# Performance work log

Measured on AMD Instinct MI355X. Metric: run time of the kernel, lower is better.

Reference implementation:

```python
import jax, jax.numpy as jnp
import numpy as np

NUM_SEQS = 64
NUM_HEADS = 32
NUM_KV_HEADS = 8
HEAD_DIM = 128
BLOCK_SIZE = 16
MAX_SEQLEN_K = 1024
BLOCKS_PER_SEQ = MAX_SEQLEN_K // BLOCK_SIZE  # 64
NUM_BLOCKS = NUM_SEQS * BLOCKS_PER_SEQ      # 4096
SCALE = 1.0 / float(np.sqrt(HEAD_DIM))
EPS = 1e-6
ROPE_BASE = 10000.0


def setup_inputs() -> dict:
    key = jax.random.key(0)
    ks = jax.random.split(key, 8)
    q = jax.random.normal(ks[0], (NUM_SEQS, NUM_HEADS * HEAD_DIM), jnp.float32)
    k = jax.random.normal(ks[1], (NUM_SEQS, NUM_KV_HEADS * HEAD_DIM), jnp.float32)
    v = jax.random.normal(ks[2], (NUM_SEQS, NUM_KV_HEADS * HEAD_DIM), jnp.float32)
    k_cache = jax.random.normal(ks[3], (NUM_BLOCKS, BLOCK_SIZE, NUM_KV_HEADS, HEAD_DIM), jnp.float32)
    v_cache = jax.random.normal(ks[4], (NUM_BLOCKS, BLOCK_SIZE, NUM_KV_HEADS, HEAD_DIM), jnp.float32)
    qw = 1.0 + 0.1 * jax.random.normal(ks[5], (HEAD_DIM,), jnp.float32)
    kw = 1.0 + 0.1 * jax.random.normal(ks[6], (HEAD_DIM,), jnp.float32)
    # neox rotary cos/sin caches over half the head dim
    inv_freq = 1.0 / (ROPE_BASE ** (jnp.arange(0, HEAD_DIM, 2, dtype=jnp.float32) / HEAD_DIM))
    ang = jnp.arange(MAX_SEQLEN_K, dtype=jnp.float32)[:, None] * inv_freq[None, :]  # [S_max, D/2]
    cos_cache = jnp.cos(ang)
    sin_cache = jnp.sin(ang)
    # decode step: each seq has context_lens tokens already; new token at position context_lens-1
    context_lens = jax.random.randint(ks[7], (NUM_SEQS,), MAX_SEQLEN_K // 2, MAX_SEQLEN_K + 1).astype(jnp.int32)
    position = context_lens - 1
    block_tables = jnp.arange(NUM_SEQS * BLOCKS_PER_SEQ, dtype=jnp.int32).reshape(NUM_SEQS, BLOCKS_PER_SEQ)
    slot_mapping = jnp.arange(NUM_SEQS, dtype=jnp.int32) * MAX_SEQLEN_K + position
    return dict(q=q, k=k, v=v, k_cache=k_cache, v_cache=v_cache, qw=qw, kw=kw,
                cos_cache=cos_cache, sin_cache=sin_cache, position=position,
                slot_mapping=slot_mapping, block_tables=block_tables, context_lens=context_lens)


def _rmsnorm(x, w):
    var = jnp.mean(x * x, axis=-1, keepdims=True)
    return x * jax.lax.rsqrt(var + EPS) * w


def _rope_neox(x, cos, sin):
    # x: [..., D]; cos/sin broadcastable to [..., D/2]
    d = x.shape[-1] // 2
    x1, x2 = x[..., :d], x[..., d:]
    return jnp.concatenate([x1 * cos - x2 * sin, x2 * cos + x1 * sin], axis=-1)


def reference(q, k, v, k_cache, v_cache, qw, kw, cos_cache, sin_cache,
              position, slot_mapping, block_tables, context_lens):
    S = q.shape[0]
    q = q.reshape(S, NUM_HEADS, HEAD_DIM)
    k = k.reshape(S, NUM_KV_HEADS, HEAD_DIM)
    v = v.reshape(S, NUM_KV_HEADS, HEAD_DIM)
    # fused qk-norm + rope
    q = _rmsnorm(q, qw)
    k = _rmsnorm(k, kw)
    cos = cos_cache[position][:, None, :]  # [S,1,D/2]
    sin = sin_cache[position][:, None, :]
    q = _rope_neox(q, cos, sin)
    k = _rope_neox(k, cos, sin)
    # reshape_and_cache: scatter new k/v tokens into the paged cache by flat slot index
    kc = k_cache.reshape(-1, NUM_KV_HEADS, HEAD_DIM).at[slot_mapping].set(k)
    vc = v_cache.reshape(-1, NUM_KV_HEADS, HEAD_DIM).at[slot_mapping].set(v)
    kc = kc.reshape(NUM_BLOCKS, BLOCK_SIZE, NUM_KV_HEADS, HEAD_DIM)
    vc = vc.reshape(NUM_BLOCKS, BLOCK_SIZE, NUM_KV_HEADS, HEAD_DIM)
    # paged attention decode: gather each sequence's blocks
    keys = kc[block_tables].reshape(S, MAX_SEQLEN_K, NUM_KV_HEADS, HEAD_DIM)
    vals = vc[block_tables].reshape(S, MAX_SEQLEN_K, NUM_KV_HEADS, HEAD_DIM)
    G = NUM_HEADS // NUM_KV_HEADS
    qg = q.reshape(S, NUM_KV_HEADS, G, HEAD_DIM)
    scores = jnp.einsum('shgd,snhd->shgn', qg, keys) * SCALE  # [S,KVH,G,N]
    valid = jnp.arange(MAX_SEQLEN_K, dtype=jnp.int32)[None, :] < context_lens[:, None]
    scores = jnp.where(valid[:, None, None, :], scores, -jnp.inf)
    probs = jax.nn.softmax(scores, axis=-1)
    out = jnp.einsum('shgn,snhd->shgd', probs, vals)  # [S,KVH,G,D]
    return out.reshape(S, NUM_HEADS * HEAD_DIM)
```

## Files before the change

kernel.cpp:

```cpp
#include <hip/hip_runtime.h>
#include <math.h>

constexpr int kNumSeqs      = 64;
constexpr int kNumHeads     = 32;
constexpr int kNumKVHeads   = 8;
constexpr int kHeadDim      = 128;
constexpr int kGQA          = 4;
constexpr int kKVBlock      = 16;
constexpr int kMaxSeqlen    = 1024;
constexpr int kBlocksPerSeq = 64;
constexpr int kPart         = 4;
constexpr int kPartSize     = 256;
constexpr float kScale      = 0.08838834764831845f;
constexpr float kEps        = 1e-6f;

constexpr size_t kAccElems = (size_t)kNumSeqs * kNumKVHeads * kPart * kGQA * kHeadDim;
constexpr size_t kMOff     = kAccElems;
constexpr size_t kLOff     = kAccElems + (size_t)kNumSeqs * kNumKVHeads * kPart * kGQA;

__launch_bounds__(256)
__global__ void paged_attn_part(
    const float* __restrict__ q,
    const float* __restrict__ k,
    const float* __restrict__ v,
    const float* __restrict__ k_cache,
    const float* __restrict__ v_cache,
    const float* __restrict__ qw,
    const float* __restrict__ kw,
    const float* __restrict__ cos_cache,
    const float* __restrict__ sin_cache,
    const int*   __restrict__ position,
    const int*   __restrict__ block_tables,
    const int*   __restrict__ context_lens,
    float* __restrict__ ws)
{
  const int bx   = blockIdx.x;
  const int s    = bx >> 5;
  const int h    = (bx >> 2) & 7;
  const int part = bx & 3;
  const int tid  = threadIdx.x;
  const int wave = tid >> 6;
  const int lane = tid & 63;

  const int ctx = context_lens[s];
  const int pos = position[s];
  const int n0  = part * kPartSize;

  float* accw = ws + ((((size_t)s * kNumKVHeads + h) * kPart + part) * kGQA) * kHeadDim;
  float* mw   = ws + kMOff + (((size_t)s * kNumKVHeads + h) * kPart + part) * kGQA;
  float* lw   = ws + kLOff + (((size_t)s * kNumKVHeads + h) * kPart + part) * kGQA;

  if (n0 >= ctx) {
    for (int e = tid; e < kGQA * kHeadDim; e += 256) accw[e] = 0.0f;
    if (tid < kGQA) { mw[tid] = -3.0e38f; lw[tid] = 0.0f; }
    return;
  }
  const int nEnd     = min(n0 + kPartSize, ctx);
  const int cnt      = nEnd - n0;
  const int posLocal = pos - n0;
  const bool haspos  = (posLocal >= 0) && (posLocal < cnt);

  __shared__ __align__(16) float sc[kGQA][kPartSize];
  __shared__ __align__(16) float q_lds[kGQA][kHeadDim];
  __shared__ __align__(16) float kn_lds[kHeadDim];
  __shared__ __align__(16) float vn_lds[kHeadDim];
  __shared__ int   bt_lds[kPartSize / kKVBlock];
  __shared__ float red[4][kGQA];
  __shared__ float mfin[kGQA];
  __shared__ float lfin[kGQA];
  __shared__ __align__(16) float outp[4][kGQA][kHeadDim];

  {
    const int g = wave;
    const float* qrow = q + (size_t)s * (kNumHeads * kHeadDim) + (h * kGQA + g) * kHeadDim;
    float x1 = qrow[lane];
    float x2 = qrow[lane + 64];
    float ss = x1 * x1 + x2 * x2;
    for (int off = 32; off >= 1; off >>= 1) ss += __shfl_xor(ss, off);
    const float r = rsqrtf(ss * (1.0f / kHeadDim) + kEps);
    x1 *= r * qw[lane];
    x2 *= r * qw[lane + 64];
    const float c  = cos_cache[pos * 64 + lane];
    const float sn = sin_cache[pos * 64 + lane];
    q_lds[g][lane]      = (x1 * c - x2 * sn) * kScale;
    q_lds[g][lane + 64] = (x2 * c + x1 * sn) * kScale;
  }
  if (wave == 0) {
    const float* krow = k + (size_t)s * (kNumKVHeads * kHeadDim) + h * kHeadDim;
    float x1 = krow[lane];
    float x2 = krow[lane + 64];
    float ss = x1 * x1 + x2 * x2;
    for (int off = 32; off >= 1; off >>= 1) ss += __shfl_xor(ss, off);
    const float r = rsqrtf(ss * (1.0f / kHeadDim) + kEps);
    x1 *= r * kw[lane];
    x2 *= r * kw[lane + 64];
    const float c  = cos_cache[pos * 64 + lane];
    const float sn = sin_cache[pos * 64 + lane];
    kn_lds[lane]      = x1 * c - x2 * sn;
    kn_lds[lane + 64] = x2 * c + x1 * sn;
  } else if (wave == 1) {
    const float* vrow = v + (size_t)s * (kNumKVHeads * kHeadDim) + h * kHeadDim;
    vn_lds[lane]      = vrow[lane];
    vn_lds[lane + 64] = vrow[lane + 64];
  } else if (wave == 2) {
    if (lane < kPartSize / kKVBlock)
      bt_lds[lane] = block_tables[s * kBlocksPerSeq + part * (kPartSize / kKVBlock) + lane];
  }
  __syncthreads();

  const int half = lane >> 5;
  const int l    = lane & 31;

  float4 qf[kGQA];
  #pragma unroll
  for (int g = 0; g < kGQA; ++g)
    qf[g] = *(const float4*)&q_lds[g][4 * l];

  const int npairs = (cnt + 1) >> 1;
  const int ppw    = (npairs + 3) >> 2;
  const int pbeg   = wave * ppw;
  const int pend   = min(pbeg + ppw, npairs);

  #pragma unroll 2
  for (int p = pbeg; p < pend; ++p) {
    const int  nl    = 2 * p + half;
    const bool valid = (nl < cnt);
    const int  nn    = valid ? nl : (cnt - 1);
    const int  blk   = bt_lds[nn >> 4];
    const float* krow =
        k_cache + (((size_t)blk * kKVBlock + (nn & 15)) * kNumKVHeads + h) * kHeadDim;
    float4 kv = *(const float4*)(krow + 4 * l);
    if (haspos && nn == posLocal) kv = *(const float4*)&kn_lds[4 * l];
    float sg[kGQA];
    #pragma unroll
    for (int g = 0; g < kGQA; ++g)
      sg[g] = qf[g].x * kv.x + qf[g].y * kv.y + qf[g].z * kv.z + qf[g].w * kv.w;
    #pragma unroll
    for (int off = 16; off >= 1; off >>= 1) {
      #pragma unroll
      for (int g = 0; g < kGQA; ++g) sg[g] += __shfl_xor(sg[g], off);
    }
    if (l == 0 && valid) {
      #pragma unroll
      for (int g = 0; g < kGQA; ++g) sc[g][nl] = sg[g];
    }
  }
  __syncthreads();

  float mg[kGQA];
  #pragma unroll
  for (int g = 0; g < kGQA; ++g) mg[g] = -3.0e38f;
  for (int n = tid; n < cnt; n += 256) {
    #pragma unroll
    for (int g = 0; g < kGQA; ++g) mg[g] = fmaxf(mg[g], sc[g][n]);
  }
  #pragma unroll
  for (int off = 32; off >= 1; off >>= 1) {
    #pragma unroll
    for (int g = 0; g < kGQA; ++g) mg[g] = fmaxf(mg[g], __shfl_xor(mg[g], off));
  }
  if (lane == 0) {
    #pragma unroll
    for (int g = 0; g < kGQA; ++g) red[wave][g] = mg[g];
  }
  __syncthreads();
  if (tid < kGQA) {
    float m = red[0][tid];
    #pragma unroll
    for (int w = 1; w < 4; ++w) m = fmaxf(m, red[w][tid]);
    mfin[tid] = m;
  }
  __syncthreads();

  float mloc[kGQA], lg[kGQA];
  #pragma unroll
  for (int g = 0; g < kGQA; ++g) { mloc[g] = mfin[g]; lg[g] = 0.0f; }
  for (int n = tid; n < cnt; n += 256) {
    #pragma unroll
    for (int g = 0; g < kGQA; ++g) {
      const float pv = __expf(sc[g][n] - mloc[g]);
      sc[g][n] = pv;
      lg[g] += pv;
    }
  }
  #pragma unroll
  for (int off = 32; off >= 1; off >>= 1) {
    #pragma unroll
    for (int g = 0; g < kGQA; ++g) lg[g] += __shfl_xor(lg[g], off);
  }
  if (lane == 0) {
    #pragma unroll
    for (int g = 0; g < kGQA; ++g) red[wave][g] = lg[g];
  }
  __syncthreads();
  if (tid < kGQA) {
    float t = 0.0f;
    #pragma unroll
    for (int w = 0; w < 4; ++w) t += red[w][tid];
    lfin[tid] = t;
  }

  float4 acc[kGQA];
  #pragma unroll
  for (int g = 0; g < kGQA; ++g) acc[g] = make_float4(0.f, 0.f, 0.f, 0.f);
  #pragma unroll 2
  for (int p = pbeg; p < pend; ++p) {
    const int  nl    = 2 * p + half;
    const bool valid = (nl < cnt);
    const int  nn    = valid ? nl : (cnt - 1);
    const int  blk   = bt_lds[nn >> 4];
    const float* vrow =
        v_cache + (((size_t)blk * kKVBlock + (nn & 15)) * kNumKVHeads + h) * kHeadDim;
    float4 vv = *(const float4*)(vrow + 4 * l);
    if (haspos && nn == posLocal) vv = *(const float4*)&vn_lds[4 * l];
    #pragma unroll
    for (int g = 0; g < kGQA; ++g) {
      const float pr = valid ? sc[g][nl] : 0.0f;
      acc[g].x += pr * vv.x;
      acc[g].y += pr * vv.y;
      acc[g].z += pr * vv.z;
      acc[g].w += pr * vv.w;
    }
  }
  #pragma unroll
  for (int g = 0; g < kGQA; ++g) {
    acc[g].x += __shfl_xor(acc[g].x, 32);
    acc[g].y += __shfl_xor(acc[g].y, 32);
    acc[g].z += __shfl_xor(acc[g].z, 32);
    acc[g].w += __shfl_xor(acc[g].w, 32);
  }
  if (half == 0) {
    #pragma unroll
    for (int g = 0; g < kGQA; ++g)
      *(float4*)&outp[wave][g][4 * l] = acc[g];
  }
  __syncthreads();

  #pragma unroll
  for (int e = tid; e < kGQA * kHeadDim; e += 256) {
    const int g = e >> 7;
    const int d = e & 127;
    float sum = 0.0f;
    #pragma unroll
    for (int w = 0; w < 4; ++w) sum += outp[w][g][d];
    accw[e] = sum;
  }
  if (tid < kGQA) { mw[tid] = mfin[tid]; lw[tid] = lfin[tid]; }
}

__launch_bounds__(128)
__global__ void paged_attn_reduce(const float* __restrict__ ws,
                                  float* __restrict__ out)
{
  const int idx = blockIdx.x;
  const int g   = idx & 3;
  const int sh  = idx >> 2;
  const int d   = threadIdx.x;

  const float* mw = ws + kMOff + (size_t)sh * (kPart * kGQA);
  const float* lw = ws + kLOff + (size_t)sh * (kPart * kGQA);

  float m[kPart];
  #pragma unroll
  for (int p = 0; p < kPart; ++p) m[p] = mw[p * kGQA + g];
  float mstar = m[0];
  #pragma unroll
  for (int p = 1; p < kPart; ++p) mstar = fmaxf(mstar, m[p]);

  float w[kPart], lstar = 0.0f;
  #pragma unroll
  for (int p = 0; p < kPart; ++p) {
    w[p] = __expf(m[p] - mstar);
    lstar += w[p] * lw[p * kGQA + g];
  }

  float o = 0.0f;
  #pragma unroll
  for (int p = 0; p < kPart; ++p) {
    const float* accp = ws + (((size_t)sh * kPart + p) * kGQA + g) * kHeadDim;
    o += w[p] * accp[d];
  }
  const int s = sh >> 3, h = sh & 7;
  out[(size_t)s * (kNumHeads * kHeadDim) + (h * kGQA + g) * kHeadDim + d] = o / lstar;
}

extern "C" void kernel_launch(void* const* d_in, const int* in_sizes, int n_in,
                              void* d_out, int out_size, void* d_ws, size_t ws_size,
                              hipStream_t stream) {
  const float* q            = (const float*)d_in[0];
  const float* k            = (const float*)d_in[1];
  const float* v            = (const float*)d_in[2];
  const float* k_cache      = (const float*)d_in[3];
  const float* v_cache      = (const float*)d_in[4];
  const float* qw           = (const float*)d_in[5];
  const float* kw           = (const float*)d_in[6];
  const float* cosc         = (const float*)d_in[7];
  const float* sinc         = (const float*)d_in[8];
  const int*   position     = (const int*)d_in[9];
  const int*   block_tables = (const int*)d_in[11];
  const int*   context_lens = (const int*)d_in[12];
  float* out                = (float*)d_out;
  float* ws                 = (float*)d_ws;

  hipLaunchKernelGGL(paged_attn_part, dim3(kNumSeqs * kNumKVHeads * kPart), dim3(256),
                     0, stream,
                     q, k, v, k_cache, v_cache, qw, kw, cosc, sinc,
                     position, block_tables, context_lens, ws);
  hipLaunchKernelGGL(paged_attn_reduce, dim3(kNumSeqs * kNumKVHeads * kGQA), dim3(kHeadDim),
                     0, stream, ws, out);
}
```

Measured before the change: 109.6 us.

## Compute QK scores one token per thread and fuse softmax in registers

```diff
diff --git a/kernel.cpp b/kernel.cpp
--- a/kernel.cpp
+++ b/kernel.cpp
@@ -55,12 +55,11 @@
     if (tid < kGQA) { mw[tid] = -3.0e38f; lw[tid] = 0.0f; }
     return;
   }
-  const int nEnd     = min(n0 + kPartSize, ctx);
-  const int cnt      = nEnd - n0;
+  const int cnt      = min(n0 + kPartSize, ctx) - n0;
   const int posLocal = pos - n0;
   const bool haspos  = (posLocal >= 0) && (posLocal < cnt);
 
-  __shared__ __align__(16) float sc[kGQA][kPartSize];
+  __shared__ __align__(16) float sc2[kPartSize][kGQA];
   __shared__ __align__(16) float q_lds[kGQA][kHeadDim];
   __shared__ __align__(16) float kn_lds[kHeadDim];
   __shared__ __align__(16) float vn_lds[kHeadDim];
@@ -108,119 +107,102 @@
   }
   __syncthreads();
 
+  const int  nl    = tid;
+  const bool validn = (nl < cnt);
+  const int  nn    = validn ? nl : (cnt - 1);
+  const bool ispos = haspos && (nn == posLocal);
+  {
+    const int blk = bt_lds[nn >> 4];
+    const float* krow =
+        k_cache + (((size_t)blk * kKVBlock + (nn & 15)) * kNumKVHeads + h) * kHeadDim;
+
+    float sg[kGQA] = {0.f, 0.f, 0.f, 0.f};
+    #pragma unroll 8
+    for (int c = 0; c < 32; ++c) {
+      float4 kv = *(const float4*)(krow + 4 * c);
+      const float4 knc = *(const float4*)&kn_lds[4 * c];
+      if (ispos) kv = knc;
+      #pragma unroll
+      for (int g = 0; g < kGQA; ++g) {
+        const float4 qc = *(const float4*)&q_lds[g][4 * c];
+        sg[g] += qc.x * kv.x + qc.y * kv.y + qc.z * kv.z + qc.w * kv.w;
+      }
+    }
+    if (!validn) {
+      #pragma unroll
+      for (int g = 0; g < kGQA; ++g) sg[g] = -3.0e38f;
+    }
+
+    float mg[kGQA];
+    #pragma unroll
+    for (int g = 0; g < kGQA; ++g) mg[g] = sg[g];
+    #pragma unroll
+    for (int off = 32; off >= 1; off >>= 1) {
+      #pragma unroll
+      for (int g = 0; g < kGQA; ++g) mg[g] = fmaxf(mg[g], __shfl_xor(mg[g], off));
+    }
+    if (lane == 0) {
+      #pragma unroll
+      for (int g = 0; g < kGQA; ++g) red[wave][g] = mg[g];
+    }
+    __syncthreads();
+    if (tid < kGQA) {
+      float m = red[0][tid];
+      #pragma unroll
+      for (int w = 1; w < 4; ++w) m = fmaxf(m, red[w][tid]);
+      mfin[tid] = m;
+    }
+    __syncthreads();
+
+    float p[kGQA], lg[kGQA];
+    #pragma unroll
+    for (int g = 0; g < kGQA; ++g) {
+      p[g]  = __expf(sg[g] - mfin[g]);
+      lg[g] = p[g];
+    }
+    *(float4*)&sc2[nl][0] = make_float4(p[0], p[1], p[2], p[3]);
+    #pragma unroll
+    for (int off = 32; off >= 1; off >>= 1) {
+      #pragma unroll
+      for (int g = 0; g < kGQA; ++g) lg[g] += __shfl_xor(lg[g], off);
+    }
+    if (lane == 0) {
+      #pragma unroll
+      for (int g = 0; g < kGQA; ++g) red[wave][g] = lg[g];
+    }
+  }
+  __syncthreads();
+  if (tid < kGQA) {
+    float t = 0.0f;
+    #pragma unroll
+    for (int w = 0; w < 4; ++w) t += red[w][tid];
+    lfin[tid] = t;
+  }
+
   const int half = lane >> 5;
   const int l    = lane & 31;
-
-  float4 qf[kGQA];
-  #pragma unroll
-  for (int g = 0; g < kGQA; ++g)
-    qf[g] = *(const float4*)&q_lds[g][4 * l];
-
   const int npairs = (cnt + 1) >> 1;
   const int ppw    = (npairs + 3) >> 2;
   const int pbeg   = wave * ppw;
   const int pend   = min(pbeg + ppw, npairs);
 
-  #pragma unroll 2
-  for (int p = pbeg; p < pend; ++p) {
-    const int  nl    = 2 * p + half;
-    const bool valid = (nl < cnt);
-    const int  nn    = valid ? nl : (cnt - 1);
-    const int  blk   = bt_lds[nn >> 4];
-    const float* krow =
-        k_cache + (((size_t)blk * kKVBlock + (nn & 15)) * kNumKVHeads + h) * kHeadDim;
-    float4 kv = *(const float4*)(krow + 4 * l);
-    if (haspos && nn == posLocal) kv = *(const float4*)&kn_lds[4 * l];
-    float sg[kGQA];
-    #pragma unroll
-    for (int g = 0; g < kGQA; ++g)
-      sg[g] = qf[g].x * kv.x + qf[g].y * kv.y + qf[g].z * kv.z + qf[g].w * kv.w;
-    #pragma unroll
-    for (int off = 16; off >= 1; off >>= 1) {
-      #pragma unroll
-      for (int g = 0; g < kGQA; ++g) sg[g] += __shfl_xor(sg[g], off);
-    }
-    if (l == 0 && valid) {
-      #pragma unroll
-      for (int g = 0; g < kGQA; ++g) sc[g][nl] = sg[g];
-    }
-  }
-  __syncthreads();
-
-  float mg[kGQA];
-  #pragma unroll
-  for (int g = 0; g < kGQA; ++g) mg[g] = -3.0e38f;
-  for (int n = tid; n < cnt; n += 256) {
-    #pragma unroll
-    for (int g = 0; g < kGQA; ++g) mg[g] = fmaxf(mg[g], sc[g][n]);
-  }
-  #pragma unroll
-  for (int off = 32; off >= 1; off >>= 1) {
-    #pragma unroll
-    for (int g = 0; g < kGQA; ++g) mg[g] = fmaxf(mg[g], __shfl_xor(mg[g], off));
-  }
-  if (lane == 0) {
-    #pragma unroll
-    for (int g = 0; g < kGQA; ++g) red[wave][g] = mg[g];
-  }
-  __syncthreads();
-  if (tid < kGQA) {
-    float m = red[0][tid];
-    #pragma unroll
-    for (int w = 1; w < 4; ++w) m = fmaxf(m, red[w][tid]);
-    mfin[tid] = m;
-  }
-  __syncthreads();
-
-  float mloc[kGQA], lg[kGQA];
-  #pragma unroll
-  for (int g = 0; g < kGQA; ++g) { mloc[g] = mfin[g]; lg[g] = 0.0f; }
-  for (int n = tid; n < cnt; n += 256) {
-    #pragma unroll
-    for (int g = 0; g < kGQA; ++g) {
-      const float pv = __expf(sc[g][n] - mloc[g]);
-      sc[g][n] = pv;
-      lg[g] += pv;
-    }
-  }
-  #pragma unroll
-  for (int off = 32; off >= 1; off >>= 1) {
-    #pragma unroll
-    for (int g = 0; g < kGQA; ++g) lg[g] += __shfl_xor(lg[g], off);
-  }
-  if (lane == 0) {
-    #pragma unroll
-    for (int g = 0; g < kGQA; ++g) red[wave][g] = lg[g];
-  }
-  __syncthreads();
-  if (tid < kGQA) {
-    float t = 0.0f;
-    #pragma unroll
-    for (int w = 0; w < 4; ++w) t += red[w][tid];
-    lfin[tid] = t;
-  }
-
   float4 acc[kGQA];
   #pragma unroll
   for (int g = 0; g < kGQA; ++g) acc[g] = make_float4(0.f, 0.f, 0.f, 0.f);
   #pragma unroll 2
   for (int p = pbeg; p < pend; ++p) {
-    const int  nl    = 2 * p + half;
-    const bool valid = (nl < cnt);
-    const int  nn    = valid ? nl : (cnt - 1);
-    const int  blk   = bt_lds[nn >> 4];
+    const int  nl2 = 2 * p + half;
+    const int  nn2 = (nl2 < cnt) ? nl2 : (cnt - 1);
+    const int  blk = bt_lds[nn2 >> 4];
     const float* vrow =
-        v_cache + (((size_t)blk * kKVBlock + (nn & 15)) * kNumKVHeads + h) * kHeadDim;
+        v_cache + (((size_t)blk * kKVBlock + (nn2 & 15)) * kNumKVHeads + h) * kHeadDim;
     float4 vv = *(const float4*)(vrow + 4 * l);
-    if (haspos && nn == posLocal) vv = *(const float4*)&vn_lds[4 * l];
-    #pragma unroll
-    for (int g = 0; g < kGQA; ++g) {
-      const float pr = valid ? sc[g][nl] : 0.0f;
-      acc[g].x += pr * vv.x;
-      acc[g].y += pr * vv.y;
-      acc[g].z += pr * vv.z;
-      acc[g].w += pr * vv.w;
-    }
+    if (haspos && nn2 == posLocal) vv = *(const float4*)&vn_lds[4 * l];
+    const float4 pr = *(const float4*)&sc2[nl2][0];
+    acc[0].x += pr.x * vv.x; acc[0].y += pr.x * vv.y; acc[0].z += pr.x * vv.z; acc[0].w += pr.x * vv.w;
+    acc[1].x += pr.y * vv.x; acc[1].y += pr.y * vv.y; acc[1].z += pr.y * vv.z; acc[1].w += pr.y * vv.w;
+    acc[2].x += pr.z * vv.x; acc[2].y += pr.z * vv.y; acc[2].z += pr.z * vv.z; acc[2].w += pr.z * vv.w;
+    acc[3].x += pr.w * vv.x; acc[3].y += pr.w * vv.y; acc[3].z += pr.w * vv.z; acc[3].w += pr.w * vv.w;
   }
   #pragma unroll
   for (int g = 0; g < kGQA; ++g) {
@@ -236,7 +218,6 @@
   }
   __syncthreads();
 
-  #pragma unroll
   for (int e = tid; e < kGQA * kHeadDim; e += 256) {
     const int g = e >> 7;
     const int d = e & 127;
```

Result: slower. 172.6 us (+57.5%).

## Batch four KV row loads per iteration and transpose score buffer layout

Applied to the files above, without the earlier changes.

```diff
diff --git a/kernel.cpp b/kernel.cpp
--- a/kernel.cpp
+++ b/kernel.cpp
@@ -55,12 +55,11 @@
     if (tid < kGQA) { mw[tid] = -3.0e38f; lw[tid] = 0.0f; }
     return;
   }
-  const int nEnd     = min(n0 + kPartSize, ctx);
-  const int cnt      = nEnd - n0;
+  const int cnt      = min(n0 + kPartSize, ctx) - n0;
   const int posLocal = pos - n0;
   const bool haspos  = (posLocal >= 0) && (posLocal < cnt);
 
-  __shared__ __align__(16) float sc[kGQA][kPartSize];
+  __shared__ __align__(16) float sc2[kPartSize][kGQA];
   __shared__ __align__(16) float q_lds[kGQA][kHeadDim];
   __shared__ __align__(16) float kn_lds[kHeadDim];
   __shared__ __align__(16) float vn_lds[kHeadDim];
@@ -115,53 +114,70 @@
   #pragma unroll
   for (int g = 0; g < kGQA; ++g)
     qf[g] = *(const float4*)&q_lds[g][4 * l];
+  const float4 knc = *(const float4*)&kn_lds[4 * l];
+  const float4 vnc = *(const float4*)&vn_lds[4 * l];
 
   const int npairs = (cnt + 1) >> 1;
-  const int ppw    = (npairs + 3) >> 2;
-  const int pbeg   = wave * ppw;
-  const int pend   = min(pbeg + ppw, npairs);
-
-  #pragma unroll 2
-  for (int p = pbeg; p < pend; ++p) {
-    const int  nl    = 2 * p + half;
-    const bool valid = (nl < cnt);
-    const int  nn    = valid ? nl : (cnt - 1);
-    const int  blk   = bt_lds[nn >> 4];
-    const float* krow =
-        k_cache + (((size_t)blk * kKVBlock + (nn & 15)) * kNumKVHeads + h) * kHeadDim;
-    float4 kv = *(const float4*)(krow + 4 * l);
-    if (haspos && nn == posLocal) kv = *(const float4*)&kn_lds[4 * l];
-    float sg[kGQA];
-    #pragma unroll
-    for (int g = 0; g < kGQA; ++g)
-      sg[g] = qf[g].x * kv.x + qf[g].y * kv.y + qf[g].z * kv.z + qf[g].w * kv.w;
+
+  for (int b = 0; wave + 16 * b < npairs; ++b) {
+    float4 kv[4];
+    int    nls[4];
+    bool   val[4];
+    #pragma unroll
+    for (int jj = 0; jj < 4; ++jj) {
+      const int  p  = wave + 16 * b + 4 * jj;
+      const bool pv = (p < npairs);
+      const int  pp = pv ? p : (npairs - 1);
+      const int  n  = 2 * pp + half;
+      const bool v  = pv && (n < cnt);
+      const int  nn = (n < cnt) ? n : (cnt - 1);
+      nls[jj] = n;
+      val[jj] = v;
+      const int blk = bt_lds[nn >> 4];
+      const float* krow =
+          k_cache + (((size_t)blk * kKVBlock + (nn & 15)) * kNumKVHeads + h) * kHeadDim;
+      kv[jj] = *(const float4*)(krow + 4 * l);
+      if (haspos && nn == posLocal) kv[jj] = knc;
+    }
+    float sg[4][kGQA];
+    #pragma unroll
+    for (int jj = 0; jj < 4; ++jj) {
+      #pragma unroll
+      for (int g = 0; g < kGQA; ++g)
+        sg[jj][g] = qf[g].x * kv[jj].x + qf[g].y * kv[jj].y +
+                    qf[g].z * kv[jj].z + qf[g].w * kv[jj].w;
+    }
     #pragma unroll
     for (int off = 16; off >= 1; off >>= 1) {
       #pragma unroll
-      for (int g = 0; g < kGQA; ++g) sg[g] += __shfl_xor(sg[g], off);
-    }
-    if (l == 0 && valid) {
-      #pragma unroll
-      for (int g = 0; g < kGQA; ++g) sc[g][nl] = sg[g];
-    }
-  }
-  __syncthreads();
-
-  float mg[kGQA];
-  #pragma unroll
-  for (int g = 0; g < kGQA; ++g) mg[g] = -3.0e38f;
-  for (int n = tid; n < cnt; n += 256) {
-    #pragma unroll
-    for (int g = 0; g < kGQA; ++g) mg[g] = fmaxf(mg[g], sc[g][n]);
-  }
-  #pragma unroll
-  for (int off = 32; off >= 1; off >>= 1) {
-    #pragma unroll
-    for (int g = 0; g < kGQA; ++g) mg[g] = fmaxf(mg[g], __shfl_xor(mg[g], off));
-  }
-  if (lane == 0) {
-    #pragma unroll
-    for (int g = 0; g < kGQA; ++g) red[wave][g] = mg[g];
+      for (int jj = 0; jj < 4; ++jj) {
+        #pragma unroll
+        for (int g = 0; g < kGQA; ++g) sg[jj][g] += __shfl_xor(sg[jj][g], off);
+      }
+    }
+    #pragma unroll
+    for (int jj = 0; jj < 4; ++jj) {
+      if (l == 0 && val[jj])
+        *(float4*)&sc2[nls[jj]][0] =
+            make_float4(sg[jj][0], sg[jj][1], sg[jj][2], sg[jj][3]);
+    }
+  }
+  __syncthreads();
+
+  float4 sv;
+  if (tid < cnt) sv = *(const float4*)&sc2[tid][0];
+  else           sv = make_float4(-3.0e38f, -3.0e38f, -3.0e38f, -3.0e38f);
+  {
+    float mg[kGQA] = {sv.x, sv.y, sv.z, sv.w};
+    #pragma unroll
+    for (int off = 32; off >= 1; off >>= 1) {
+      #pragma unroll
+      for (int g = 0; g < kGQA; ++g) mg[g] = fmaxf(mg[g], __shfl_xor(mg[g], off));
+    }
+    if (lane == 0) {
+      #pragma unroll
+      for (int g = 0; g < kGQA; ++g) red[wave][g] = mg[g];
+    }
   }
   __syncthreads();
   if (tid < kGQA) {
@@ -172,25 +188,23 @@
   }
   __syncthreads();
 
-  float mloc[kGQA], lg[kGQA];
-  #pragma unroll
-  for (int g = 0; g < kGQA; ++g) { mloc[g] = mfin[g]; lg[g] = 0.0f; }
-  for (int n = tid; n < cnt; n += 256) {
-    #pragma unroll
-    for (int g = 0; g < kGQA; ++g) {
-      const float pv = __expf(sc[g][n] - mloc[g]);
-      sc[g][n] = pv;
-      lg[g] += pv;
-    }
-  }
-  #pragma unroll
-  for (int off = 32; off >= 1; off >>= 1) {
-    #pragma unroll
-    for (int g = 0; g < kGQA; ++g) lg[g] += __shfl_xor(lg[g], off);
-  }
-  if (lane == 0) {
-    #pragma unroll
-    for (int g = 0; g < kGQA; ++g) red[wave][g] = lg[g];
+  {
+    float4 pv4;
+    pv4.x = __expf(sv.x - mfin[0]);
+    pv4.y = __expf(sv.y - mfin[1]);
+    pv4.z = __expf(sv.z - mfin[2]);
+    pv4.w = __expf(sv.w - mfin[3]);
+    *(float4*)&sc2[tid][0] = pv4;
+    float lg[kGQA] = {pv4.x, pv4.y, pv4.z, pv4.w};
+    #pragma unroll
+    for (int off = 32; off >= 1; off >>= 1) {
+      #pragma unroll
+      for (int g = 0; g < kGQA; ++g) lg[g] += __shfl_xor(lg[g], off);
+    }
+    if (lane == 0) {
+      #pragma unroll
+      for (int g = 0; g < kGQA; ++g) red[wave][g] = lg[g];
+    }
   }
   __syncthreads();
   if (tid < kGQA) {
@@ -203,23 +217,33 @@
   float4 acc[kGQA];
   #pragma unroll
   for (int g = 0; g < kGQA; ++g) acc[g] = make_float4(0.f, 0.f, 0.f, 0.f);
-  #pragma unroll 2
-  for (int p = pbeg; p < pend; ++p) {
-    const int  nl    = 2 * p + half;
-    const bool valid = (nl < cnt);
-    const int  nn    = valid ? nl : (cnt - 1);
-    const int  blk   = bt_lds[nn >> 4];
-    const float* vrow =
-        v_cache + (((size_t)blk * kKVBlock + (nn & 15)) * kNumKVHeads + h) * kHeadDim;
-    float4 vv = *(const float4*)(vrow + 4 * l);
-    if (haspos && nn == posLocal) vv = *(const float4*)&vn_lds[4 * l];
-    #pragma unroll
-    for (int g = 0; g < kGQA; ++g) {
-      const float pr = valid ? sc[g][nl] : 0.0f;
-      acc[g].x += pr * vv.x;
-      acc[g].y += pr * vv.y;
-      acc[g].z += pr * vv.z;
-      acc[g].w += pr * vv.w;
+  for (int b = 0; wave + 16 * b < npairs; ++b) {
+    float4 vv[4];
+    float4 pr[4];
+    #pragma unroll
+    for (int jj = 0; jj < 4; ++jj) {
+      const int  p  = wave + 16 * b + 4 * jj;
+      const bool pv = (p < npairs);
+      const int  pp = pv ? p : (npairs - 1);
+      const int  n  = 2 * pp + half;
+      const int  nn = (n < cnt) ? n : (cnt - 1);
+      const int  blk = bt_lds[nn >> 4];
+      const float* vrow =
+          v_cache + (((size_t)blk * kKVBlock + (nn & 15)) * kNumKVHeads + h) * kHeadDim;
+      vv[jj] = *(const float4*)(vrow + 4 * l);
+      if (haspos && nn == posLocal) vv[jj] = vnc;
+      pr[jj] = pv ? *(const float4*)&sc2[n][0] : make_float4(0.f, 0.f, 0.f, 0.f);
+    }
+    #pragma unroll
+    for (int jj = 0; jj < 4; ++jj) {
+      acc[0].x += pr[jj].x * vv[jj].x; acc[0].y += pr[jj].x * vv[jj].y;
+      acc[0].z += pr[jj].x * vv[jj].z; acc[0].w += pr[jj].x * vv[jj].w;
+      acc[1].x += pr[jj].y * vv[jj].x; acc[1].y += pr[jj].y * vv[jj].y;
+      acc[1].z += pr[jj].y * vv[jj].z; acc[1].w += pr[jj].y * vv[jj].w;
+      acc[2].x += pr[jj].z * vv[jj].x; acc[2].y += pr[jj].z * vv[jj].y;
+      acc[2].z += pr[jj].z * vv[jj].z; acc[2].w += pr[jj].z * vv[jj].w;
+      acc[3].x += pr[jj].w * vv[jj].x; acc[3].y += pr[jj].w * vv[jj].y;
+      acc[3].z += pr[jj].w * vv[jj].z; acc[3].w += pr[jj].w * vv[jj].w;
     }
   }
   #pragma unroll
@@ -236,7 +260,6 @@
   }
   __syncthreads();
 
-  #pragma unroll
   for (int e = tid; e < kGQA * kHeadDim; e += 256) {
     const int g = e >> 7;
     const int d = e & 127;
```

After: 99.25 us. 1.1x faster.
